# Performance work log

Measured on AMD Instinct MI355X. Metric: run time of the kernel, lower is better.

The kernel has to match this reference:

```python
import jax, jax.numpy as jnp
import numpy as np

B, SQ, SK, DQ, DK, DV = 8, 2048, 2048, 128, 128, 128

def setup_inputs() -> dict:
    key = jax.random.key(0)
    k1, k2, k3, k4 = jax.random.split(key, 4)
    # xavier_uniform for weights [DQ, DK]
    limit = float(np.sqrt(6.0 / (DQ + DK)))
    weights = jax.random.uniform(k4, (DQ, DK), jnp.float32, -limit, limit)
    return {
        "query": jax.random.normal(k1, (B, SQ, DQ), jnp.float32),
        "key": jax.random.normal(k2, (B, SK, DK), jnp.float32),
        "value": jax.random.normal(k3, (B, SK, DV), jnp.float32),
        "weights": weights,
    }

def reference(query, key, value, weights):
    # score = (query @ W) @ key^T, computed as two GEMMs (faithful math, no [B,Sq,Dk,Sk] blow-up)
    qw = jnp.einsum('bqd,dk->bqk', query, weights)          # [B,SQ,DK]
    score = jnp.einsum('bqk,bsk->bqs', qw, key)             # [B,SQ,SK]
    weight = jax.nn.softmax(score, axis=-1)                 # dropout=0 -> identity
    out = jnp.einsum('bqs,bsv->bqv', weight, value)         # [B,SQ,DV]
    return out, weight
```

## Files before the change

### kernel.cpp

```cpp
#include <hip/hip_runtime.h>

#define B_  8
#define SQ_ 2048
#define SK_ 2048
#define D_  128

typedef float  f32x4 __attribute__((ext_vector_type(4)));
typedef short  s16x8 __attribute__((ext_vector_type(8)));
typedef __bf16 b16x8 __attribute__((ext_vector_type(8)));

__device__ __forceinline__ f32x4 mfma16(s16x8 a, s16x8 b, f32x4 c) {
    return __builtin_amdgcn_mfma_f32_16x16x32_bf16(
        __builtin_bit_cast(b16x8, a), __builtin_bit_cast(b16x8, b), c, 0, 0, 0);
}

__device__ __forceinline__ unsigned int bfpack(float a, float b) {
    return (__float_as_uint(a) >> 16) | (__float_as_uint(b) & 0xFFFF0000u);
}

__device__ __forceinline__ void split4(const float4 v, uint2& hi, uint2& lo) {
    float hx = __uint_as_float(__float_as_uint(v.x) & 0xFFFF0000u);
    float hy = __uint_as_float(__float_as_uint(v.y) & 0xFFFF0000u);
    float hz = __uint_as_float(__float_as_uint(v.z) & 0xFFFF0000u);
    float hw = __uint_as_float(__float_as_uint(v.w) & 0xFFFF0000u);
    hi.x = bfpack(v.x, v.y); hi.y = bfpack(v.z, v.w);
    lo.x = bfpack(v.x - hx, v.y - hy); lo.y = bfpack(v.z - hz, v.w - hw);
}

union U8 { unsigned int u[4]; s16x8 v; };

__global__ __launch_bounds__(256) void k1_qw(const float* __restrict__ q,
                                             const float* __restrict__ w,
                                             float* __restrict__ qw) {
    __shared__ float Ws[D_ * D_];
    const int tid = threadIdx.x;
    const int rowbase = blockIdx.x * 64;
    #pragma unroll
    for (int t = 0; t < 16; ++t) {
        int i4 = t * 256 + tid;
        ((float4*)Ws)[i4] = ((const float4*)w)[i4];
    }
    __syncthreads();
    const int mg = tid >> 4, cg = tid & 15;
    const int c0 = cg * 8;
    const float* qrow[4];
    #pragma unroll
    for (int i = 0; i < 4; ++i)
        qrow[i] = q + (size_t)(rowbase + mg * 4 + i) * D_;
    float acc[4][8];
    #pragma unroll
    for (int i = 0; i < 4; ++i)
        #pragma unroll
        for (int j = 0; j < 8; ++j) acc[i][j] = 0.0f;
    for (int d0 = 0; d0 < D_; d0 += 16) {
        float qr[4][16];
        #pragma unroll
        for (int i = 0; i < 4; ++i)
            #pragma unroll
            for (int c4 = 0; c4 < 4; ++c4)
                *(float4*)&qr[i][c4 * 4] = *(const float4*)(qrow[i] + d0 + c4 * 4);
        #pragma unroll
        for (int dd = 0; dd < 16; ++dd) {
            const int d = d0 + dd;
            float4 w0 = *(const float4*)&Ws[d * D_ + c0];
            float4 w1 = *(const float4*)&Ws[d * D_ + c0 + 4];
            #pragma unroll
            for (int i = 0; i < 4; ++i) {
                float a = qr[i][dd];
                acc[i][0] += a * w0.x; acc[i][1] += a * w0.y;
                acc[i][2] += a * w0.z; acc[i][3] += a * w0.w;
                acc[i][4] += a * w1.x; acc[i][5] += a * w1.y;
                acc[i][6] += a * w1.z; acc[i][7] += a * w1.w;
            }
        }
    }
    #pragma unroll
    for (int i = 0; i < 4; ++i) {
        float* dst = qw + (size_t)(rowbase + mg * 4 + i) * D_ + c0;
        *(float4*)dst       = make_float4(acc[i][0], acc[i][1], acc[i][2], acc[i][3]);
        *(float4*)(dst + 4) = make_float4(acc[i][4], acc[i][5], acc[i][6], acc[i][7]);
    }
}

__global__ __launch_bounds__(256) void k2_score_stats(
        const float* __restrict__ qw, const float* __restrict__ key,
        float* __restrict__ S, float* __restrict__ m_ws, float* __restrict__ l_ws) {
    __shared__ unsigned short Khi[64 * 136];
    __shared__ unsigned short Klo[64 * 136];
    __shared__ float s_m[2][32], s_l[2][32];

    const int tid  = threadIdx.x;
    const int b    = blockIdx.y;
    const int m0   = blockIdx.x * 32;
    const int w    = tid >> 6, lane = tid & 63;
    const int mw   = w >> 1,  nw   = w & 1;
    const int quad = lane >> 4, l15 = lane & 15;

    const float* arow = qw + ((size_t)b * SQ_ + m0 + mw * 16 + l15) * D_;
    s16x8 a_hi[4], a_lo[4];
    #pragma unroll
    for (int k0 = 0; k0 < 4; ++k0) {
        const float* p = arow + k0 * 32 + quad * 8;
        float4 v0 = *(const float4*)p;
        float4 v1 = *(const float4*)(p + 4);
        uint2 h0, l0, h1, l1;
        split4(v0, h0, l0); split4(v1, h1, l1);
        U8 H, L;
        H.u[0] = h0.x; H.u[1] = h0.y; H.u[2] = h1.x; H.u[3] = h1.y;
        L.u[0] = l0.x; L.u[1] = l0.y; L.u[2] = l1.x; L.u[3] = l1.y;
        a_hi[k0] = H.v; a_lo[k0] = L.v;
    }

    float rm[4], rl[4];
    #pragma unroll
    for (int r = 0; r < 4; ++r) { rm[r] = -1e30f; rl[r] = 0.0f; }

    const int rb0 = nw * 32 + l15, rb1 = nw * 32 + 16 + l15;

    for (int t = 0; t < SK_ / 64; ++t) {
        const int n0 = t * 64;
        __syncthreads();
        const float* Kg = key + ((size_t)b * SK_ + n0) * D_;
        #pragma unroll
        for (int it = 0; it < 8; ++it) {
            int idx = it * 256 + tid;
            int r = idx >> 5, c4 = idx & 31;
            float4 v = ((const float4*)(Kg + (size_t)r * D_))[c4];
            uint2 h, l; split4(v, h, l);
            unsigned int* ph = (unsigned int*)Khi + r * 68 + c4 * 2;
            unsigned int* pl = (unsigned int*)Klo + r * 68 + c4 * 2;
            ph[0] = h.x; ph[1] = h.y; pl[0] = l.x; pl[1] = l.y;
        }
        __syncthreads();

        f32x4 acc0 = {0.f, 0.f, 0.f, 0.f}, acc1 = {0.f, 0.f, 0.f, 0.f};
        #pragma unroll
        for (int k0 = 0; k0 < 4; ++k0) {
            int c8 = (k0 * 4 + quad) * 8;
            s16x8 bh0 = *(const s16x8*)&Khi[rb0 * 136 + c8];
            s16x8 bl0 = *(const s16x8*)&Klo[rb0 * 136 + c8];
            s16x8 bh1 = *(const s16x8*)&Khi[rb1 * 136 + c8];
            s16x8 bl1 = *(const s16x8*)&Klo[rb1 * 136 + c8];
            acc0 = mfma16(a_hi[k0], bh0, acc0);
            acc0 = mfma16(a_lo[k0], bh0, acc0);
            acc0 = mfma16(a_hi[k0], bl0, acc0);
            acc1 = mfma16(a_hi[k0], bh1, acc1);
            acc1 = mfma16(a_lo[k0], bh1, acc1);
            acc1 = mfma16(a_hi[k0], bl1, acc1);
        }

        float* Sp = S + ((size_t)b * SQ_ + m0 + mw * 16 + quad * 4) * SK_
                      + n0 + nw * 32 + l15;
        #pragma unroll
        for (int r = 0; r < 4; ++r) {
            Sp[(size_t)r * SK_]      = acc0[r];
            Sp[(size_t)r * SK_ + 16] = acc1[r];
        }

        #pragma unroll
        for (int r = 0; r < 4; ++r) {
            float tm = fmaxf(acc0[r], acc1[r]);
            tm = fmaxf(tm, __shfl_xor(tm, 1, 64));
            tm = fmaxf(tm, __shfl_xor(tm, 2, 64));
            tm = fmaxf(tm, __shfl_xor(tm, 4, 64));
            tm = fmaxf(tm, __shfl_xor(tm, 8, 64));
            float ts = __expf(acc0[r] - tm) + __expf(acc1[r] - tm);
            ts += __shfl_xor(ts, 1, 64);
            ts += __shfl_xor(ts, 2, 64);
            ts += __shfl_xor(ts, 4, 64);
            ts += __shfl_xor(ts, 8, 64);
            float nm = fmaxf(rm[r], tm);
            rl[r] = rl[r] * __expf(rm[r] - nm) + ts * __expf(tm - nm);
            rm[r] = nm;
        }
    }

    if (l15 == 0) {
        #pragma unroll
        for (int r = 0; r < 4; ++r) {
            s_m[nw][mw * 16 + quad * 4 + r] = rm[r];
            s_l[nw][mw * 16 + quad * 4 + r] = rl[r];
        }
    }
    __syncthreads();
    if (tid < 32) {
        float ma = s_m[0][tid], mb = s_m[1][tid];
        float M = fmaxf(ma, mb);
        float L = s_l[0][tid] * __expf(ma - M) + s_l[1][tid] * __expf(mb - M);
        m_ws[(size_t)b * SQ_ + m0 + tid] = M;
        l_ws[(size_t)b * SQ_ + m0 + tid] = L;
    }
}

__global__ __launch_bounds__(256) void k3_pv(float* __restrict__ Wgt,
        const float* __restrict__ V, float* __restrict__ O,
        const float* __restrict__ m_ws, const float* __restrict__ l_ws) {
    __shared__ unsigned short Pt[32 * 72];
    __shared__ unsigned short Vt[128 * 72];

    const int tid  = threadIdx.x;
    const int b    = blockIdx.y;
    const int m0   = blockIdx.x * 32;
    const int w    = tid >> 6, lane = tid & 63;
    const int mw   = w >> 1,  nw   = w & 1;
    const int quad = lane >> 4, l15 = lane & 15;

    const int pr = tid >> 3, pc = tid & 7;
    const float m_r  = m_ws[(size_t)b * SQ_ + m0 + pr];
    const float invl = 1.0f / l_ws[(size_t)b * SQ_ + m0 + pr];
    float* Prow = Wgt + ((size_t)b * SQ_ + m0 + pr) * SK_;

    const int vn4 = tid >> 3, vk2 = tid & 7;
    const float* Vb = V + (size_t)b * SK_ * D_;

    f32x4 acc[4];
    #pragma unroll
    for (int nf = 0; nf < 4; ++nf) acc[nf] = (f32x4){0.f, 0.f, 0.f, 0.f};

    for (int kt = 0; kt < SK_; kt += 64) {
        __syncthreads();
        #pragma unroll
        for (int e = 0; e < 2; ++e) {
            int c4 = pc * 2 + e;
            float4 s4 = ((const float4*)(Prow + kt))[c4];
            float4 p4;
            p4.x = __expf(s4.x - m_r) * invl;
            p4.y = __expf(s4.y - m_r) * invl;
            p4.z = __expf(s4.z - m_r) * invl;
            p4.w = __expf(s4.w - m_r) * invl;
            ((float4*)(Prow + kt))[c4] = p4;
            unsigned int* pp = (unsigned int*)Pt + pr * 36 + c4 * 2;
            pp[0] = bfpack(p4.x, p4.y);
            pp[1] = bfpack(p4.z, p4.w);
        }
        #pragma unroll
        for (int i = 0; i < 4; ++i) {
            int kp = vk2 * 4 + i;
            const float* vp = Vb + (size_t)(kt + kp * 2) * D_ + vn4 * 4;
            float4 va  = *(const float4*)vp;
            float4 vb4 = *(const float4*)(vp + D_);
            unsigned int* qv = (unsigned int*)Vt;
            qv[(vn4 * 4 + 0) * 36 + kp] = bfpack(va.x, vb4.x);
            qv[(vn4 * 4 + 1) * 36 + kp] = bfpack(va.y, vb4.y);
            qv[(vn4 * 4 + 2) * 36 + kp] = bfpack(va.z, vb4.z);
            qv[(vn4 * 4 + 3) * 36 + kp] = bfpack(va.w, vb4.w);
        }
        __syncthreads();
        #pragma unroll
        for (int k0 = 0; k0 < 2; ++k0) {
            int c8 = (k0 * 4 + quad) * 8;
            s16x8 af = *(const s16x8*)&Pt[(mw * 16 + l15) * 72 + c8];
            #pragma unroll
            for (int nf = 0; nf < 4; ++nf) {
                s16x8 bf = *(const s16x8*)&Vt[(nw * 64 + nf * 16 + l15) * 72 + c8];
                acc[nf] = mfma16(af, bf, acc[nf]);
            }
        }
    }

    float* Op = O + ((size_t)b * SQ_ + m0 + mw * 16 + quad * 4) * D_ + nw * 64 + l15;
    #pragma unroll
    for (int nf = 0; nf < 4; ++nf)
        #pragma unroll
        for (int r = 0; r < 4; ++r)
            Op[(size_t)r * D_ + nf * 16] = acc[nf][r];
}

extern "C" void kernel_launch(void* const* d_in, const int* in_sizes, int n_in,
                              void* d_out, int out_size, void* d_ws, size_t ws_size,
                              hipStream_t stream) {
    const float* q = (const float*)d_in[0];
    const float* k = (const float*)d_in[1];
    const float* v = (const float*)d_in[2];
    const float* w = (const float*)d_in[3];
    float* out    = (float*)d_out;
    float* weight = out + (size_t)B_ * SQ_ * D_;
    float* qw     = out;
    float* m_ws   = (float*)d_ws;
    float* l_ws   = m_ws + (size_t)B_ * SQ_;

    k1_qw<<<(B_ * SQ_) / 64, 256, 0, stream>>>(q, w, qw);
    k2_score_stats<<<dim3(SQ_ / 32, B_), 256, 0, stream>>>(qw, k, weight, m_ws, l_ws);
    k3_pv<<<dim3(SQ_ / 32, B_), 256, 0, stream>>>(weight, v, out, m_ws, l_ws);
}
```

Before: 442.3 us.

## Split score GEMM into 2D tiles, add separate row-stats pass, shrink PV tile

The score kernel no longer loops over all keys per 32-row block carrying online softmax stats. It is now a 2D-tiled GEMM over 64x64 output tiles, each loading one K tile once, which gives far more blocks and more reuse of A registers. Row max and sum move into a new kernel that rereads the full score matrix (an extra 128MB read). The PV kernel uses 16-row blocks to double the grid size, at the cost of reloading V more times.

Result: faster. 384.3 us (-13.1%).

```diff
diff --git a/kernel.cpp b/kernel.cpp
--- a/kernel.cpp
+++ b/kernel.cpp
@@ -82,130 +82,131 @@
     }
 }
 
-__global__ __launch_bounds__(256) void k2_score_stats(
+__global__ __launch_bounds__(256) void k2_score(
         const float* __restrict__ qw, const float* __restrict__ key,
-        float* __restrict__ S, float* __restrict__ m_ws, float* __restrict__ l_ws) {
+        float* __restrict__ S) {
     __shared__ unsigned short Khi[64 * 136];
     __shared__ unsigned short Klo[64 * 136];
-    __shared__ float s_m[2][32], s_l[2][32];
 
     const int tid  = threadIdx.x;
-    const int b    = blockIdx.y;
-    const int m0   = blockIdx.x * 32;
+    const int b    = blockIdx.z;
+    const int m0   = blockIdx.y * 64;
+    const int n0   = blockIdx.x * 64;
     const int w    = tid >> 6, lane = tid & 63;
     const int mw   = w >> 1,  nw   = w & 1;
     const int quad = lane >> 4, l15 = lane & 15;
 
-    const float* arow = qw + ((size_t)b * SQ_ + m0 + mw * 16 + l15) * D_;
-    s16x8 a_hi[4], a_lo[4];
+    #pragma unroll
+    for (int it = 0; it < 8; ++it) {
+        int idx = it * 256 + tid;
+        int r = idx >> 5, c4 = idx & 31;
+        float4 v = ((const float4*)(key + ((size_t)b * SK_ + n0 + r) * D_))[c4];
+        uint2 h, l; split4(v, h, l);
+        unsigned int* ph = (unsigned int*)Khi + r * 68 + c4 * 2;
+        unsigned int* pl = (unsigned int*)Klo + r * 68 + c4 * 2;
+        ph[0] = h.x; ph[1] = h.y; pl[0] = l.x; pl[1] = l.y;
+    }
+
+    s16x8 a_hi[2][4], a_lo[2][4];
+    #pragma unroll
+    for (int rt = 0; rt < 2; ++rt) {
+        const float* ar = qw + ((size_t)b * SQ_ + m0 + mw * 32 + rt * 16 + l15) * D_;
+        #pragma unroll
+        for (int k0 = 0; k0 < 4; ++k0) {
+            const float* p = ar + k0 * 32 + quad * 8;
+            float4 v0 = *(const float4*)p;
+            float4 v1 = *(const float4*)(p + 4);
+            uint2 h0, l0, h1, l1;
+            split4(v0, h0, l0); split4(v1, h1, l1);
+            U8 H, L;
+            H.u[0] = h0.x; H.u[1] = h0.y; H.u[2] = h1.x; H.u[3] = h1.y;
+            L.u[0] = l0.x; L.u[1] = l0.y; L.u[2] = l1.x; L.u[3] = l1.y;
+            a_hi[rt][k0] = H.v; a_lo[rt][k0] = L.v;
+        }
+    }
+    __syncthreads();
+
+    f32x4 acc[2][2];
+    #pragma unroll
+    for (int rt = 0; rt < 2; ++rt)
+        #pragma unroll
+        for (int ct = 0; ct < 2; ++ct) acc[rt][ct] = (f32x4){0.f, 0.f, 0.f, 0.f};
+
     #pragma unroll
     for (int k0 = 0; k0 < 4; ++k0) {
-        const float* p = arow + k0 * 32 + quad * 8;
-        float4 v0 = *(const float4*)p;
-        float4 v1 = *(const float4*)(p + 4);
-        uint2 h0, l0, h1, l1;
-        split4(v0, h0, l0); split4(v1, h1, l1);
-        U8 H, L;
-        H.u[0] = h0.x; H.u[1] = h0.y; H.u[2] = h1.x; H.u[3] = h1.y;
-        L.u[0] = l0.x; L.u[1] = l0.y; L.u[2] = l1.x; L.u[3] = l1.y;
-        a_hi[k0] = H.v; a_lo[k0] = L.v;
-    }
-
-    float rm[4], rl[4];
-    #pragma unroll
-    for (int r = 0; r < 4; ++r) { rm[r] = -1e30f; rl[r] = 0.0f; }
-
-    const int rb0 = nw * 32 + l15, rb1 = nw * 32 + 16 + l15;
-
-    for (int t = 0; t < SK_ / 64; ++t) {
-        const int n0 = t * 64;
-        __syncthreads();
-        const float* Kg = key + ((size_t)b * SK_ + n0) * D_;
-        #pragma unroll
-        for (int it = 0; it < 8; ++it) {
-            int idx = it * 256 + tid;
-            int r = idx >> 5, c4 = idx & 31;
-            float4 v = ((const float4*)(Kg + (size_t)r * D_))[c4];
-            uint2 h, l; split4(v, h, l);
-            unsigned int* ph = (unsigned int*)Khi + r * 68 + c4 * 2;
-            unsigned int* pl = (unsigned int*)Klo + r * 68 + c4 * 2;
-            ph[0] = h.x; ph[1] = h.y; pl[0] = l.x; pl[1] = l.y;
-        }
-        __syncthreads();
-
-        f32x4 acc0 = {0.f, 0.f, 0.f, 0.f}, acc1 = {0.f, 0.f, 0.f, 0.f};
-        #pragma unroll
-        for (int k0 = 0; k0 < 4; ++k0) {
-            int c8 = (k0 * 4 + quad) * 8;
-            s16x8 bh0 = *(const s16x8*)&Khi[rb0 * 136 + c8];
-            s16x8 bl0 = *(const s16x8*)&Klo[rb0 * 136 + c8];
-            s16x8 bh1 = *(const s16x8*)&Khi[rb1 * 136 + c8];
-            s16x8 bl1 = *(const s16x8*)&Klo[rb1 * 136 + c8];
-            acc0 = mfma16(a_hi[k0], bh0, acc0);
-            acc0 = mfma16(a_lo[k0], bh0, acc0);
-            acc0 = mfma16(a_hi[k0], bl0, acc0);
-            acc1 = mfma16(a_hi[k0], bh1, acc1);
-            acc1 = mfma16(a_lo[k0], bh1, acc1);
-            acc1 = mfma16(a_hi[k0], bl1, acc1);
-        }
-
-        float* Sp = S + ((size_t)b * SQ_ + m0 + mw * 16 + quad * 4) * SK_
+        const int c8 = (k0 * 4 + quad) * 8;
+        s16x8 bh[2], bl[2];
+        #pragma unroll
+        for (int ct = 0; ct < 2; ++ct) {
+            int rb = nw * 32 + ct * 16 + l15;
+            bh[ct] = *(const s16x8*)&Khi[rb * 136 + c8];
+            bl[ct] = *(const s16x8*)&Klo[rb * 136 + c8];
+        }
+        #pragma unroll
+        for (int rt = 0; rt < 2; ++rt)
+            #pragma unroll
+            for (int ct = 0; ct < 2; ++ct) {
+                acc[rt][ct] = mfma16(a_hi[rt][k0], bh[ct], acc[rt][ct]);
+                acc[rt][ct] = mfma16(a_lo[rt][k0], bh[ct], acc[rt][ct]);
+                acc[rt][ct] = mfma16(a_hi[rt][k0], bl[ct], acc[rt][ct]);
+            }
+    }
+
+    #pragma unroll
+    for (int rt = 0; rt < 2; ++rt) {
+        float* Sp = S + ((size_t)b * SQ_ + m0 + mw * 32 + rt * 16 + quad * 4) * SK_
                       + n0 + nw * 32 + l15;
         #pragma unroll
-        for (int r = 0; r < 4; ++r) {
-            Sp[(size_t)r * SK_]      = acc0[r];
-            Sp[(size_t)r * SK_ + 16] = acc1[r];
-        }
-
-        #pragma unroll
-        for (int r = 0; r < 4; ++r) {
-            float tm = fmaxf(acc0[r], acc1[r]);
-            tm = fmaxf(tm, __shfl_xor(tm, 1, 64));
-            tm = fmaxf(tm, __shfl_xor(tm, 2, 64));
-            tm = fmaxf(tm, __shfl_xor(tm, 4, 64));
-            tm = fmaxf(tm, __shfl_xor(tm, 8, 64));
-            float ts = __expf(acc0[r] - tm) + __expf(acc1[r] - tm);
-            ts += __shfl_xor(ts, 1, 64);
-            ts += __shfl_xor(ts, 2, 64);
-            ts += __shfl_xor(ts, 4, 64);
-            ts += __shfl_xor(ts, 8, 64);
-            float nm = fmaxf(rm[r], tm);
-            rl[r] = rl[r] * __expf(rm[r] - nm) + ts * __expf(tm - nm);
-            rm[r] = nm;
-        }
-    }
-
-    if (l15 == 0) {
-        #pragma unroll
-        for (int r = 0; r < 4; ++r) {
-            s_m[nw][mw * 16 + quad * 4 + r] = rm[r];
-            s_l[nw][mw * 16 + quad * 4 + r] = rl[r];
-        }
-    }
-    __syncthreads();
-    if (tid < 32) {
-        float ma = s_m[0][tid], mb = s_m[1][tid];
-        float M = fmaxf(ma, mb);
-        float L = s_l[0][tid] * __expf(ma - M) + s_l[1][tid] * __expf(mb - M);
-        m_ws[(size_t)b * SQ_ + m0 + tid] = M;
-        l_ws[(size_t)b * SQ_ + m0 + tid] = L;
+        for (int r = 0; r < 4; ++r)
+            #pragma unroll
+            for (int ct = 0; ct < 2; ++ct)
+                Sp[(size_t)r * SK_ + ct * 16] = acc[rt][ct][r];
+    }
+}
+
+__global__ __launch_bounds__(256) void k2b_stats(const float* __restrict__ S,
+        float* __restrict__ m_ws, float* __restrict__ l_ws) {
+    const int row  = blockIdx.x * 4 + (threadIdx.x >> 6);
+    const int lane = threadIdx.x & 63;
+    const float4* p = (const float4*)(S + (size_t)row * SK_);
+    float4 x[8];
+    #pragma unroll
+    for (int i = 0; i < 8; ++i) x[i] = p[i * 64 + lane];
+
+    float m = -1e30f;
+    #pragma unroll
+    for (int i = 0; i < 8; ++i)
+        m = fmaxf(m, fmaxf(fmaxf(x[i].x, x[i].y), fmaxf(x[i].z, x[i].w)));
+    #pragma unroll
+    for (int off = 32; off; off >>= 1) m = fmaxf(m, __shfl_xor(m, off, 64));
+
+    float s = 0.f;
+    #pragma unroll
+    for (int i = 0; i < 8; ++i)
+        s += __expf(x[i].x - m) + __expf(x[i].y - m) +
+             __expf(x[i].z - m) + __expf(x[i].w - m);
+    #pragma unroll
+    for (int off = 32; off; off >>= 1) s += __shfl_xor(s, off, 64);
+
+    if (lane == 0) {
+        m_ws[row] = m;
+        l_ws[row] = s;
     }
 }
 
 __global__ __launch_bounds__(256) void k3_pv(float* __restrict__ Wgt,
         const float* __restrict__ V, float* __restrict__ O,
         const float* __restrict__ m_ws, const float* __restrict__ l_ws) {
-    __shared__ unsigned short Pt[32 * 72];
+    __shared__ unsigned short Pt[16 * 72];
     __shared__ unsigned short Vt[128 * 72];
 
     const int tid  = threadIdx.x;
     const int b    = blockIdx.y;
-    const int m0   = blockIdx.x * 32;
+    const int m0   = blockIdx.x * 16;
     const int w    = tid >> 6, lane = tid & 63;
-    const int mw   = w >> 1,  nw   = w & 1;
     const int quad = lane >> 4, l15 = lane & 15;
 
-    const int pr = tid >> 3, pc = tid & 7;
+    const int pr = tid >> 4, pc = tid & 15;
     const float m_r  = m_ws[(size_t)b * SQ_ + m0 + pr];
     const float invl = 1.0f / l_ws[(size_t)b * SQ_ + m0 + pr];
     float* Prow = Wgt + ((size_t)b * SQ_ + m0 + pr) * SK_;
@@ -213,23 +214,21 @@
     const int vn4 = tid >> 3, vk2 = tid & 7;
     const float* Vb = V + (size_t)b * SK_ * D_;
 
-    f32x4 acc[4];
-    #pragma unroll
-    for (int nf = 0; nf < 4; ++nf) acc[nf] = (f32x4){0.f, 0.f, 0.f, 0.f};
+    f32x4 acc[2];
+    acc[0] = (f32x4){0.f, 0.f, 0.f, 0.f};
+    acc[1] = (f32x4){0.f, 0.f, 0.f, 0.f};
 
     for (int kt = 0; kt < SK_; kt += 64) {
         __syncthreads();
-        #pragma unroll
-        for (int e = 0; e < 2; ++e) {
-            int c4 = pc * 2 + e;
-            float4 s4 = ((const float4*)(Prow + kt))[c4];
+        {
+            float4 s4 = ((const float4*)(Prow + kt))[pc];
             float4 p4;
             p4.x = __expf(s4.x - m_r) * invl;
             p4.y = __expf(s4.y - m_r) * invl;
             p4.z = __expf(s4.z - m_r) * invl;
             p4.w = __expf(s4.w - m_r) * invl;
-            ((float4*)(Prow + kt))[c4] = p4;
-            unsigned int* pp = (unsigned int*)Pt + pr * 36 + c4 * 2;
+            ((float4*)(Prow + kt))[pc] = p4;
+            unsigned int* pp = (unsigned int*)Pt + pr * 36 + pc * 2;
             pp[0] = bfpack(p4.x, p4.y);
             pp[1] = bfpack(p4.z, p4.w);
         }
@@ -249,18 +248,18 @@
         #pragma unroll
         for (int k0 = 0; k0 < 2; ++k0) {
             int c8 = (k0 * 4 + quad) * 8;
-            s16x8 af = *(const s16x8*)&Pt[(mw * 16 + l15) * 72 + c8];
-            #pragma unroll
-            for (int nf = 0; nf < 4; ++nf) {
-                s16x8 bf = *(const s16x8*)&Vt[(nw * 64 + nf * 16 + l15) * 72 + c8];
+            s16x8 af = *(const s16x8*)&Pt[l15 * 72 + c8];
+            #pragma unroll
+            for (int nf = 0; nf < 2; ++nf) {
+                s16x8 bf = *(const s16x8*)&Vt[(w * 32 + nf * 16 + l15) * 72 + c8];
                 acc[nf] = mfma16(af, bf, acc[nf]);
             }
         }
     }
 
-    float* Op = O + ((size_t)b * SQ_ + m0 + mw * 16 + quad * 4) * D_ + nw * 64 + l15;
-    #pragma unroll
-    for (int nf = 0; nf < 4; ++nf)
+    float* Op = O + ((size_t)b * SQ_ + m0 + quad * 4) * D_ + w * 32 + l15;
+    #pragma unroll
+    for (int nf = 0; nf < 2; ++nf)
         #pragma unroll
         for (int r = 0; r < 4; ++r)
             Op[(size_t)r * D_ + nf * 16] = acc[nf][r];
@@ -280,6 +279,7 @@
     float* l_ws   = m_ws + (size_t)B_ * SQ_;
 
     k1_qw<<<(B_ * SQ_) / 64, 256, 0, stream>>>(q, w, qw);
-    k2_score_stats<<<dim3(SQ_ / 32, B_), 256, 0, stream>>>(qw, k, weight, m_ws, l_ws);
-    k3_pv<<<dim3(SQ_ / 32, B_), 256, 0, stream>>>(weight, v, out, m_ws, l_ws);
-}
+    k2_score<<<dim3(SK_ / 64, SQ_ / 64, B_), 256, 0, stream>>>(qw, k, weight);
+    k2b_stats<<<(B_ * SQ_) / 4, 256, 0, stream>>>(weight, m_ws, l_ws);
+    k3_pv<<<dim3(SQ_ / 16, B_), 256, 0, stream>>>(weight, v, out, m_ws, l_ws);
+}
```
